# Kernel tuning notes

Measured on AMD Instinct MI355X. Metric: run time of the kernel, lower is better.

The kernel has to match this reference:

```python
import jax, jax.numpy as jnp
import numpy as np

# Model dims (match init_kwargs / Mamba2 defaults)
D_MODEL = 1024
D_STATE = 128
D_CONV = 4
EXPAND = 2
HEADDIM = 64
NGROUPS = 1
D_INNER = EXPAND * D_MODEL            # 2048
NHEADS = D_INNER // HEADDIM           # 32
D_IN_PROJ = 2 * D_INNER + 2 * NGROUPS * D_STATE + NHEADS  # 4384 (d_mlp == 0)
CONV_DIM = D_INNER + 2 * NGROUPS * D_STATE                 # 2304
BATCH = 2
SEQLEN = 512
EPS = 1e-5


def _silu(x):
    return x * jax.nn.sigmoid(x)


def setup_inputs() -> dict:
    key = jax.random.key(0)
    ks = jax.random.split(key, 8)
    u = jax.random.normal(ks[0], (BATCH, SEQLEN, D_MODEL), jnp.float32)
    W_in = jax.random.normal(ks[1], (D_IN_PROJ, D_MODEL), jnp.float32) * (D_MODEL ** -0.5)
    conv_w = jax.random.normal(ks[2], (CONV_DIM, 1, D_CONV), jnp.float32) * (D_CONV ** -0.5)
    conv_b = jnp.zeros((CONV_DIM,), jnp.float32)
    # dt_bias init as in the torch module (inverse-softplus of dt in [dt_min, dt_max])
    dt = jnp.exp(jax.random.uniform(ks[3], (NHEADS,), jnp.float32)
                 * (np.log(0.1) - np.log(0.001)) + np.log(0.001))
    dt = jnp.clip(dt, 1e-4, None)
    dt_bias = dt + jnp.log(-jnp.expm1(-dt))
    A_log = jnp.log(jax.random.uniform(ks[4], (NHEADS,), jnp.float32, minval=1.0, maxval=16.0))
    D_param = jnp.ones((NHEADS,), jnp.float32)
    norm_w = jnp.ones((D_INNER,), jnp.float32)
    W_out = jax.random.normal(ks[5], (D_MODEL, D_INNER), jnp.float32) * (D_INNER ** -0.5)
    return dict(u=u, W_in=W_in, conv_w=conv_w, conv_b=conv_b, dt_bias=dt_bias,
                A_log=A_log, D_param=D_param, norm_w=norm_w, W_out=W_out)


def reference(u, W_in, conv_w, conv_b, dt_bias, A_log, D_param, norm_w, W_out):
    B, L, _ = u.shape
    # in_proj (no bias): [B,L,d_in_proj]
    zxbcdt = jnp.einsum('bld,ed->ble', u, W_in)
    z = zxbcdt[..., :D_INNER]
    xBC = zxbcdt[..., D_INNER:D_INNER + CONV_DIM]
    dt = zxbcdt[..., D_INNER + CONV_DIM:]          # [B,L,H]

    # causal depthwise conv1d (pad left d_conv-1 == conv padding + slice in torch)
    xc = jnp.transpose(xBC, (0, 2, 1))             # [B,C,L]
    xc = jax.lax.conv_general_dilated(
        xc, conv_w, window_strides=(1,), padding=[(D_CONV - 1, 0)],
        dimension_numbers=('NCH', 'OIH', 'NCH'), feature_group_count=CONV_DIM)
    xc = xc + conv_b[None, :, None]
    xBC = _silu(jnp.transpose(xc, (0, 2, 1)))      # [B,L,C]

    x = xBC[..., :D_INNER].reshape(B, L, NHEADS, HEADDIM)
    Bv = xBC[..., D_INNER:D_INNER + NGROUPS * D_STATE].reshape(B, L, NGROUPS, D_STATE)
    Cv = xBC[..., D_INNER + NGROUPS * D_STATE:].reshape(B, L, NGROUPS, D_STATE)

    A = -jnp.exp(A_log)                            # [H]
    dt = jax.nn.softplus(dt + dt_bias)             # [B,L,H]

    def step(state, inp):
        dt_t, x_t, B_t, C_t = inp                  # [B,H],[B,H,P],[B,G,N],[B,G,N]
        dA = jnp.exp(dt_t * A)                     # [B,H]
        dBx = jnp.einsum('bh,bgn,bhp->bhpn', dt_t, B_t, x_t)
        state = state * dA[:, :, None, None] + dBx
        y = jnp.einsum('bhpn,bgn->bhp', state, C_t) + D_param[:, None] * x_t
        return state, y

    state0 = jnp.zeros((B, NHEADS, HEADDIM, D_STATE), u.dtype)
    xs = (jnp.moveaxis(dt, 1, 0), jnp.moveaxis(x, 1, 0),
          jnp.moveaxis(Bv, 1, 0), jnp.moveaxis(Cv, 1, 0))
    _, ys = jax.lax.scan(step, state0, xs)         # ys: [L,B,H,P]
    y = jnp.moveaxis(ys, 0, 1).reshape(B, L, D_INNER)

    # RMSNormGated, norm_before_gate=False: gate first, then rmsnorm
    yg = y * _silu(z)
    yn = yg * jax.lax.rsqrt(jnp.mean(yg * yg, axis=-1, keepdims=True) + EPS) * norm_w

    return jnp.einsum('bld,ed->ble', yn, W_out)    # out_proj, no bias
```

## Files before the change

kernel.cpp:

```cpp
#include <hip/hip_runtime.h>
#include <hip/hip_bf16.h>

#define D_MODEL   1024
#define D_STATE   128
#define D_INNER   2048
#define NHEADS    32
#define HEADDIM   64
#define D_IN_PROJ 4384
#define NPROJ_PAD 4480
#define CONV_DIM  2304
#define BATCH     2
#define SEQLEN    512
#define M_TOKENS  (BATCH*SEQLEN)
#define EPS       1e-5f
#define LC        64
#define NCH       (SEQLEN/LC)

typedef __bf16 bf16x8 __attribute__((ext_vector_type(8)));
typedef float  f32x4  __attribute__((ext_vector_type(4)));

__device__ __forceinline__ ushort f2bf(float f) {
  union { float f; unsigned int i; } v; v.f = f;
  unsigned int x = v.i;
  return (ushort)((x + 0x7fffu + ((x >> 16) & 1u)) >> 16);
}
__device__ __forceinline__ float bf2f(ushort u) {
  union { unsigned int i; float f; } v; v.i = ((unsigned int)u) << 16; return v.f;
}

__device__ __forceinline__ void gload_lds16u(const ushort* g, ushort* l) {
  __builtin_amdgcn_global_load_lds(
      (const __attribute__((address_space(1))) void*)g,
      (__attribute__((address_space(3))) void*)l, 16, 0, 0);
}

__device__ __forceinline__ void cvt8(const float* __restrict__ s,
                                     ushort* __restrict__ d, int i) {
  const float4 a = *(const float4*)(s + i);
  const float4 b = *(const float4*)(s + i + 4);
  uint4 v;
  v.x = (unsigned)f2bf(a.x) | ((unsigned)f2bf(a.y) << 16);
  v.y = (unsigned)f2bf(a.z) | ((unsigned)f2bf(a.w) << 16);
  v.z = (unsigned)f2bf(b.x) | ((unsigned)f2bf(b.y) << 16);
  v.w = (unsigned)f2bf(b.z) | ((unsigned)f2bf(b.w) << 16);
  *(uint4*)(d + i) = v;
}
__global__ __launch_bounds__(256) void cvt3z(const float* __restrict__ s0, ushort* __restrict__ d0, int n0,
                                             const float* __restrict__ s1, ushort* __restrict__ d1, int n1,
                                             const float* __restrict__ s2, ushort* __restrict__ d2, int n2,
                                             const float* __restrict__ nw,
                                             float* __restrict__ zout, int n3,
                                             float* __restrict__ zsum, int n4) {
  const int i = (blockIdx.x * 256 + threadIdx.x) * 8;
  if (i < n0)           cvt8(s0, d0, i);
  else if (i < n0 + n1) cvt8(s1, d1, i - n0);
  else if (i < n0 + n1 + n2) {
    const int j = i - n0 - n1;
    const int k = j & (D_INNER - 1);
    const float4 a = *(const float4*)(s2 + j);
    const float4 b = *(const float4*)(s2 + j + 4);
    const float4 wa = *(const float4*)(nw + k);
    const float4 wb = *(const float4*)(nw + k + 4);
    uint4 v;
    v.x = (unsigned)f2bf(a.x * wa.x) | ((unsigned)f2bf(a.y * wa.y) << 16);
    v.y = (unsigned)f2bf(a.z * wa.z) | ((unsigned)f2bf(a.w * wa.w) << 16);
    v.z = (unsigned)f2bf(b.x * wb.x) | ((unsigned)f2bf(b.y * wb.y) << 16);
    v.w = (unsigned)f2bf(b.z * wb.z) | ((unsigned)f2bf(b.w * wb.w) << 16);
    *(uint4*)(d2 + j) = v;
  } else if (i < n0 + n1 + n2 + n3) {
    const int j = i - n0 - n1 - n2;
    const float4 z = {0.f, 0.f, 0.f, 0.f};
    *(float4*)(zout + j) = z;
    *(float4*)(zout + j + 4) = z;
  } else if (i < n0 + n1 + n2 + n3 + n4) {
    const int j = i - n0 - n1 - n2 - n3;
    const float4 z = {0.f, 0.f, 0.f, 0.f};
    *(float4*)(zsum + j) = z;
    *(float4*)(zsum + j + 4) = z;
  }
}

template <int BM, int BN, int PK>
__global__ __launch_bounds__(256) void gemm_tile(const ushort* __restrict__ A,
                                                 const ushort* __restrict__ Bt,
                                                 ushort* __restrict__ C,
                                                 int Nreal, int K, int ldc) {
  constexpr int WM = BM / 2, WN = BN / 2, FM = WM / 16, FN = WN / 16;
  constexpr int LA = BM * 4 / 256, LB = BN * 4 / 256;
  __shared__ ushort As[PK * BM * 32];
  __shared__ ushort Bs[PK * BN * 32];
  const int tid = threadIdx.x, lane = tid & 63, wave = tid >> 6;
  const int r16 = lane & 15, q = lane >> 4;
  const int wm = wave & 1, wn = wave >> 1;
  const int m0 = blockIdx.y * BM, n0 = blockIdx.x * BN;

  f32x4 acc[FM][FN] = {};

  for (int k0 = 0; k0 < K; k0 += 32 * PK) {
    __syncthreads();
    #pragma unroll
    for (int pp = 0; pp < PK; ++pp) {
      #pragma unroll
      for (int it = 0; it < LA; ++it) {
        const int idx = it * 256 + tid;
        gload_lds16u(A + (size_t)(m0 + (idx >> 2)) * K + k0 + pp * 32 + (idx & 3) * 8,
                     As + pp * BM * 32 + (it * 256 + wave * 64) * 8);
      }
      #pragma unroll
      for (int it = 0; it < LB; ++it) {
        const int idx = it * 256 + tid;
        gload_lds16u(Bt + (size_t)(n0 + (idx >> 2)) * K + k0 + pp * 32 + (idx & 3) * 8,
                     Bs + pp * BN * 32 + (it * 256 + wave * 64) * 8);
      }
    }
    __syncthreads();

    #pragma unroll
    for (int pp = 0; pp < PK; ++pp) {
      bf16x8 af[FM], bfr[FN];
      #pragma unroll
      for (int i = 0; i < FM; ++i)
        af[i] = *(const bf16x8*)(const void*)(As + pp * BM * 32 + (wm * WM + i * 16 + r16) * 32 + q * 8);
      #pragma unroll
      for (int j = 0; j < FN; ++j)
        bfr[j] = *(const bf16x8*)(const void*)(Bs + pp * BN * 32 + (wn * WN + j * 16 + r16) * 32 + q * 8);
      #pragma unroll
      for (int i = 0; i < FM; ++i)
        #pragma unroll
        for (int j = 0; j < FN; ++j)
          acc[i][j] = __builtin_amdgcn_mfma_f32_16x16x32_bf16(af[i], bfr[j], acc[i][j], 0, 0, 0);
    }
  }

  #pragma unroll
  for (int i = 0; i < FM; ++i) {
    const int row = m0 + wm * WM + i * 16 + q * 4;
    #pragma unroll
    for (int j = 0; j < FN; ++j) {
      const int col = n0 + wn * WN + j * 16 + r16;
      if (col < Nreal) {
        #pragma unroll
        for (int r = 0; r < 4; ++r)
          C[(size_t)(row + r) * ldc + col] = f2bf(acc[i][j][r]);
      }
    }
  }
}

__global__ __launch_bounds__(256) void gemm_sk(const ushort* __restrict__ A,
                                               const ushort* __restrict__ Bt,
                                               float* __restrict__ C,
                                               const float* __restrict__ sumsq,
                                               int Khalf, int ldab, int ldc) {
  __shared__ ushort As[4 * 64 * 32];
  __shared__ ushort Bs[4 * 64 * 32];
  const int tid = threadIdx.x, lane = tid & 63, wave = tid >> 6;
  const int r16 = lane & 15, q = lane >> 4;
  const int wm = wave & 1, wn = wave >> 1;
  const int m0 = blockIdx.y * 64, n0 = blockIdx.x * 64;
  const int kb = blockIdx.z * Khalf;

  f32x4 acc[2][2] = {};
  for (int k0 = 0; k0 < Khalf; k0 += 128) {
    __syncthreads();
    #pragma unroll
    for (int pp = 0; pp < 4; ++pp) {
      gload_lds16u(A + (size_t)(m0 + (tid >> 2)) * ldab + kb + k0 + pp * 32 + (tid & 3) * 8,
                   As + pp * 64 * 32 + (tid & ~63) * 8);
      gload_lds16u(Bt + (size_t)(n0 + (tid >> 2)) * ldab + kb + k0 + pp * 32 + (tid & 3) * 8,
                   Bs + pp * 64 * 32 + (tid & ~63) * 8);
    }
    __syncthreads();

    #pragma unroll
    for (int pp = 0; pp < 4; ++pp) {
      bf16x8 af[2], bfr[2];
      #pragma unroll
      for (int i = 0; i < 2; ++i)
        af[i] = *(const bf16x8*)(const void*)(As + pp * 64 * 32 + (wm * 32 + i * 16 + r16) * 32 + q * 8);
      #pragma unroll
      for (int j = 0; j < 2; ++j)
        bfr[j] = *(const bf16x8*)(const void*)(Bs + pp * 64 * 32 + (wn * 32 + j * 16 + r16) * 32 + q * 8);
      #pragma unroll
      for (int i = 0; i < 2; ++i)
        #pragma unroll
        for (int j = 0; j < 2; ++j)
          acc[i][j] = __builtin_amdgcn_mfma_f32_16x16x32_bf16(af[i], bfr[j], acc[i][j], 0, 0, 0);
    }
  }

  #pragma unroll
  for (int i = 0; i < 2; ++i) {
    const int row = m0 + wm * 32 + i * 16 + q * 4;
    float rms[4];
    #pragma unroll
    for (int r = 0; r < 4; ++r)
      rms[r] = rsqrtf(sumsq[row + r] * (1.f / D_INNER) + EPS);
    #pragma unroll
    for (int j = 0; j < 2; ++j) {
      const int col = n0 + wn * 32 + j * 16 + r16;
      #pragma unroll
      for (int r = 0; r < 4; ++r)
        unsafeAtomicAdd(&C[(size_t)(row + r) * ldc + col], acc[i][j][r] * rms[r]);
    }
  }
}

__global__ __launch_bounds__(256) void conv_dt(const ushort* __restrict__ zx,
                                               const float* __restrict__ cw,
                                               const float* __restrict__ cb,
                                               ushort* __restrict__ xbc,
                                               const float* __restrict__ dt_bias,
                                               const float* __restrict__ A_log,
                                               float* __restrict__ dts,
                                               float* __restrict__ csum) {
  const int blk = blockIdx.x;
  if (blk < 1152) {
    const int g  = blk / 9;
    const int c  = (blk % 9) * 256 + threadIdx.x;
    const int b  = g >> 6;
    const int t0 = (g & 63) * 8;
    const float4 w4 = *(const float4*)(cw + c * 4);
    const float bias = cb[c];
    const ushort* col = zx + (size_t)(b * SEQLEN) * D_IN_PROJ + D_INNER + c;
    float win[11];
    #pragma unroll
    for (int k = 0; k < 11; ++k) {
      const int t = t0 - 3 + k;
      win[k] = (t >= 0) ? bf2f(col[(size_t)t * D_IN_PROJ]) : 0.f;
    }
    #pragma unroll
    for (int i = 0; i < 8; ++i) {
      float a = bias;
      a = fmaf(win[i],     w4.x, a);
      a = fmaf(win[i + 1], w4.y, a);
      a = fmaf(win[i + 2], w4.z, a);
      a = fmaf(win[i + 3], w4.w, a);
      const float s = a / (1.f + __expf(-a));
      xbc[(size_t)(b * SEQLEN + t0 + i) * CONV_DIM + c] = f2bf(s);
    }
  } else {
    const int bh = blk - 1152;
    const int b = bh >> 5, h = bh & 31;
    const int wave = threadIdx.x >> 6, lane = threadIdx.x & 63;
    const float dtb = dt_bias[h];
    const float An  = -__expf(A_log[h]);
    for (int cc = wave; cc < NCH; cc += 4) {
      const int t = cc * LC + lane;
      const float raw = bf2f(zx[(size_t)(b * SEQLEN + t) * D_IN_PROJ + (D_INNER + CONV_DIM) + h]) + dtb;
      const float sp = (raw > 20.f) ? raw : log1pf(__expf(raw));
      float x = sp * An;
      #pragma unroll
      for (int off = 1; off < 64; off <<= 1) {
        const float v = __shfl_up(x, off);
        if (lane >= off) x += v;
      }
      dts[(size_t)bh * SEQLEN + t]  = sp;
      csum[(size_t)bh * SEQLEN + t] = x;
    }
  }
}

__global__ __launch_bounds__(256) void chunk_intra(const ushort* __restrict__ xbc,
                                                   const float* __restrict__ dts,
                                                   const float* __restrict__ csum,
                                                   ushort* __restrict__ Yi,
                                                   ushort* __restrict__ dS) {
  const int blk = blockIdx.x;
  const int c = blk & 7, h = (blk >> 3) & 31, b = blk >> 8;
  const int bh = b * 32 + h;
  const int tid = threadIdx.x, lane = tid & 63, wave = tid >> 6;
  const int r16 = lane & 15, q = lane >> 4;

  __shared__ ushort Ml[64 * 72];
  __shared__ ushort Xt[64 * 72];
  __shared__ ushort Bw[128 * 72];
  __shared__ float dtl[LC], csl[LC];

  if (tid < LC) {
    dtl[tid] = dts[(size_t)bh * SEQLEN + c * LC + tid];
    csl[tid] = csum[(size_t)bh * SEQLEN + c * LC + tid];
  }
  __syncthreads();
  const float cs63 = csl[LC - 1];

  const ushort* rowbase = xbc + (size_t)(b * SEQLEN + c * LC) * CONV_DIM;
  const ushort* Cp = rowbase + (size_t)(wave * 16 + r16) * CONV_DIM + D_INNER + 128 + q * 8;
  const ushort* Bp = rowbase + (size_t)r16 * CONV_DIM + D_INNER + q * 8;
  f32x4 g[4] = {};
  #pragma unroll
  for (int kk = 0; kk < 4; ++kk) {
    const bf16x8 a = *(const bf16x8*)(const void*)(Cp + kk * 32);
    #pragma unroll
    for (int j = 0; j < 4; ++j) {
      const bf16x8 bb = *(const bf16x8*)(const void*)(Bp + (size_t)j * 16 * CONV_DIM + kk * 32);
      g[j] = __builtin_amdgcn_mfma_f32_16x16x32_bf16(a, bb, g[j], 0, 0, 0);
    }
  }
  float cst[4];
  #pragma unroll
  for (int r = 0; r < 4; ++r) cst[r] = csl[wave * 16 + q * 4 + r];
  #pragma unroll
  for (int j = 0; j < 4; ++j) {
    const int s = j * 16 + r16;
    const float ds_ = dtl[s], css = csl[s];
    #pragma unroll
    for (int r = 0; r < 4; ++r) {
      const int t = wave * 16 + q * 4 + r;
      const float v = (s <= t) ? g[j][r] * ds_ * __expf(cst[r] - css) : 0.f;
      Ml[t * 72 + s] = f2bf(v);
    }
  }

  const ushort* xb = rowbase + h * HEADDIM;
  #pragma unroll
  for (int i = 0; i < 16; ++i) {
    const int idx = i * 256 + tid;
    const int s = idx >> 6, p = idx & 63;
    Xt[p * 72 + s] = xb[(size_t)s * CONV_DIM + p];
  }
  const ushort* Bb = rowbase + D_INNER;
  #pragma unroll
  for (int i = 0; i < 32; ++i) {
    const int idx = i * 256 + tid;
    const int s = idx >> 7, n = idx & 127;
    const float w = dtl[s] * __expf(cs63 - csl[s]);
    Bw[n * 72 + s] = f2bf(bf2f(Bb[(size_t)s * CONV_DIM + n]) * w);
  }
  __syncthreads();

  f32x4 accY[4] = {};
  f32x4 accS[2][4] = {};
  #pragma unroll
  for (int kk = 0; kk < 2; ++kk) {
    const bf16x8 am = *(const bf16x8*)(const void*)(Ml + (wave * 16 + r16) * 72 + kk * 32 + q * 8);
    const bf16x8 a0 = *(const bf16x8*)(const void*)(Bw + (wave * 32 + r16) * 72 + kk * 32 + q * 8);
    const bf16x8 a1 = *(const bf16x8*)(const void*)(Bw + (wave * 32 + 16 + r16) * 72 + kk * 32 + q * 8);
    #pragma unroll
    for (int j = 0; j < 4; ++j) {
      const bf16x8 bx = *(const bf16x8*)(const void*)(Xt + (j * 16 + r16) * 72 + kk * 32 + q * 8);
      accY[j]    = __builtin_amdgcn_mfma_f32_16x16x32_bf16(am, bx, accY[j], 0, 0, 0);
      accS[0][j] = __builtin_amdgcn_mfma_f32_16x16x32_bf16(a0, bx, accS[0][j], 0, 0, 0);
      accS[1][j] = __builtin_amdgcn_mfma_f32_16x16x32_bf16(a1, bx, accS[1][j], 0, 0, 0);
    }
  }

  ushort* Yp = Yi + (size_t)blk * 4096;
  #pragma unroll
  for (int j = 0; j < 4; ++j)
    #pragma unroll
    for (int r = 0; r < 4; ++r)
      Yp[(wave * 16 + q * 4 + r) * 64 + j * 16 + r16] = f2bf(accY[j][r]);

  ushort* Sp = dS + (size_t)blk * 8192;
  #pragma unroll
  for (int u = 0; u < 2; ++u)
    #pragma unroll
    for (int j = 0; j < 4; ++j)
      #pragma unroll
      for (int r = 0; r < 4; ++r)
        Sp[(wave * 32 + u * 16 + q * 4 + r) * 64 + j * 16 + r16] = f2bf(accS[u][j][r]);
}

__global__ __launch_bounds__(256) void chunk_inter(const ushort* __restrict__ xbc,
                                                   const ushort* __restrict__ dS,
                                                   const ushort* __restrict__ Yi,
                                                   const ushort* __restrict__ zx,
                                                   const float* __restrict__ csum,
                                                   const float* __restrict__ Dp,
                                                   ushort* __restrict__ yn,
                                                   float* __restrict__ sumsq) {
  const int blk = blockIdx.x;
  const int c = blk & 7, h = (blk >> 3) & 31, b = blk >> 8;
  const int bh = b * 32 + h;
  const int tid = threadIdx.x, lane = tid & 63, wave = tid >> 6;
  const int r16 = lane & 15, q = lane >> 4;

  __shared__ ushort Stile[64 * 132];

  const int p  = tid & 63;
  const int n0 = (tid >> 6) * 32;
  float S[32] = {};
  float w = 1.f;
  for (int cp = c - 1; cp >= 0; --cp) {
    const ushort* dp = dS + ((size_t)bh * 8 + cp) * 8192 + (size_t)n0 * 64 + p;
    #pragma unroll
    for (int j = 0; j < 32; ++j)
      S[j] = fmaf(w, bf2f(dp[(size_t)j * 64]), S[j]);
    w *= __expf(csum[(size_t)bh * SEQLEN + cp * LC + (LC - 1)]);
  }
  #pragma unroll
  for (int j = 0; j < 16; ++j) {
    const unsigned v = (unsigned)f2bf(S[2 * j]) | ((unsigned)f2bf(S[2 * j + 1]) << 16);
    *(unsigned*)&Stile[p * 132 + n0 + 2 * j] = v;
  }
  __syncthreads();

  const ushort* rowbase = xbc + (size_t)(b * SEQLEN + c * LC) * CONV_DIM;
  const ushort* Cp = rowbase + (size_t)(wave * 16 + r16) * CONV_DIM + D_INNER + 128 + q * 8;
  f32x4 acc[4] = {};
  #pragma unroll
  for (int kk = 0; kk < 4; ++kk) {
    const bf16x8 a = *(const bf16x8*)(const void*)(Cp + kk * 32);
    #pragma unroll
    for (int j = 0; j < 4; ++j) {
      const bf16x8 bb = *(const bf16x8*)(const void*)(Stile + (j * 16 + r16) * 132 + kk * 32 + q * 8);
      acc[j] = __builtin_amdgcn_mfma_f32_16x16x32_bf16(a, bb, acc[j], 0, 0, 0);
    }
  }

  const float Dh = Dp[h];
  const ushort* Yp = Yi + (size_t)blk * 4096;
  float sc[4], ssq[4] = {0.f, 0.f, 0.f, 0.f};
  #pragma unroll
  for (int r = 0; r < 4; ++r)
    sc[r] = __expf(csum[(size_t)bh * SEQLEN + c * LC + wave * 16 + q * 4 + r]);
  #pragma unroll
  for (int j = 0; j < 4; ++j) {
    const int col = j * 16 + r16;
    #pragma unroll
    for (int r = 0; r < 4; ++r) {
      const int t = wave * 16 + q * 4 + r;
      const size_t row = (size_t)(b * SEQLEN + c * LC + t);
      const float xv = bf2f(xbc[row * CONV_DIM + h * HEADDIM + col]);
      const float yv = acc[j][r] * sc[r] + bf2f(Yp[t * 64 + col]) + Dh * xv;
      const float z  = bf2f(zx[row * D_IN_PROJ + h * HEADDIM + col]);
      const float yg = yv * (z / (1.f + __expf(-z)));
      yn[row * D_INNER + h * HEADDIM + col] = f2bf(yg);
      ssq[r] = fmaf(yg, yg, ssq[r]);
    }
  }
  #pragma unroll
  for (int o = 1; o < 16; o <<= 1) {
    #pragma unroll
    for (int r = 0; r < 4; ++r) ssq[r] += __shfl_xor(ssq[r], o);
  }
  if (r16 == 0) {
    #pragma unroll
    for (int r = 0; r < 4; ++r) {
      const int t = wave * 16 + q * 4 + r;
      unsafeAtomicAdd(&sumsq[b * SEQLEN + c * LC + t], ssq[r]);
    }
  }
}

extern "C" void kernel_launch(void* const* d_in, const int* in_sizes, int n_in,
                              void* d_out, int out_size, void* d_ws, size_t ws_size,
                              hipStream_t stream) {
  const float* u       = (const float*)d_in[0];
  const float* W_in    = (const float*)d_in[1];
  const float* conv_w  = (const float*)d_in[2];
  const float* conv_b  = (const float*)d_in[3];
  const float* dt_bias = (const float*)d_in[4];
  const float* A_log   = (const float*)d_in[5];
  const float* D_par   = (const float*)d_in[6];
  const float* norm_w  = (const float*)d_in[7];
  const float* W_out   = (const float*)d_in[8];
  float* out = (float*)d_out;

  char* ws = (char*)d_ws;
  ushort* zx      = (ushort*)ws;
  ushort* xbc     = (ushort*)(ws + 8978432);
  float*  sumsq   = (float*)(ws + 13697024);
  ushort* yn      = (ushort*)(ws + 13701120);
  ushort* u_bf    = (ushort*)(ws + 17895424);
  ushort* Win_bf  = (ushort*)(ws + 19992576);
  ushort* Yi      = (ushort*)(ws + 17895424);
  ushort* Wout_bf = (ushort*)(ws + 28971008);
  float*  dts     = (float*)(ws + 33165312);
  float*  csum    = (float*)(ws + 33296384);
  ushort* dS      = (ushort*)(ws + 33427456);

  const int n_u = M_TOKENS * D_MODEL, n_wi = D_IN_PROJ * D_MODEL, n_wo = D_MODEL * D_INNER;
  const int n_out = M_TOKENS * D_MODEL, n_ss = M_TOKENS;
  const int n_tot = n_u + n_wi + n_wo + n_out + n_ss;
  cvt3z<<<(n_tot + 2047) / 2048, 256, 0, stream>>>(
      u, u_bf, n_u, W_in, Win_bf, n_wi, W_out, Wout_bf, n_wo, norm_w,
      out, n_out, sumsq, n_ss);

  gemm_tile<128, 64, 4><<<dim3(NPROJ_PAD / 64, M_TOKENS / 128), 256, 0, stream>>>(
      u_bf, Win_bf, zx, D_IN_PROJ, D_MODEL, D_IN_PROJ);
  conv_dt<<<1152 + 64, 256, 0, stream>>>(zx, conv_w, conv_b, xbc,
                                         dt_bias, A_log, dts, csum);

  chunk_intra<<<BATCH * NHEADS * NCH, 256, 0, stream>>>(xbc, dts, csum, Yi, dS);
  chunk_inter<<<BATCH * NHEADS * NCH, 256, 0, stream>>>(xbc, dS, Yi, zx,
                                                        csum, D_par, yn, sumsq);

  gemm_sk<<<dim3(D_MODEL / 64, M_TOKENS / 64, 2), 256, 0, stream>>>(
      yn, Wout_bf, out, sumsq, D_INNER / 2, D_INNER, D_MODEL);
}
```

Baseline: 164.2 us.

## Double-buffer LDS staging in both GEMM kernels to overlap loads with MFMA

Both the in-projection and out-projection GEMMs switch from a single-stage LDS fill (4 sub-tiles of K=32, two barriers per step) to a two-buffer ping-pong of 2 sub-tiles each. The next K=64 slab is issued into the other buffer before the MFMAs run on the current one, and each iteration needs only one barrier. The aim is to hide global-to-LDS latency behind compute. LDS footprint stays the same, but each iteration covers half as much K, so there are twice as many loop trips.

```diff
diff --git a/kernel.cpp b/kernel.cpp
--- a/kernel.cpp
+++ b/kernel.cpp
@@ -80,15 +80,15 @@
   }
 }
 
-template <int BM, int BN, int PK>
+template <int BM, int BN>
 __global__ __launch_bounds__(256) void gemm_tile(const ushort* __restrict__ A,
                                                  const ushort* __restrict__ Bt,
                                                  ushort* __restrict__ C,
                                                  int Nreal, int K, int ldc) {
   constexpr int WM = BM / 2, WN = BN / 2, FM = WM / 16, FN = WN / 16;
   constexpr int LA = BM * 4 / 256, LB = BN * 4 / 256;
-  __shared__ ushort As[PK * BM * 32];
-  __shared__ ushort Bs[PK * BN * 32];
+  __shared__ ushort As[2 * 2 * BM * 32];
+  __shared__ ushort Bs[2 * 2 * BN * 32];
   const int tid = threadIdx.x, lane = tid & 63, wave = tid >> 6;
   const int r16 = lane & 15, q = lane >> 4;
   const int wm = wave & 1, wn = wave >> 1;
@@ -96,34 +96,39 @@
 
   f32x4 acc[FM][FN] = {};
 
-  for (int k0 = 0; k0 < K; k0 += 32 * PK) {
-    __syncthreads();
-    #pragma unroll
-    for (int pp = 0; pp < PK; ++pp) {
+  auto stage = [&](int buf, int k0) {
+    #pragma unroll
+    for (int pp = 0; pp < 2; ++pp) {
       #pragma unroll
       for (int it = 0; it < LA; ++it) {
         const int idx = it * 256 + tid;
         gload_lds16u(A + (size_t)(m0 + (idx >> 2)) * K + k0 + pp * 32 + (idx & 3) * 8,
-                     As + pp * BM * 32 + (it * 256 + wave * 64) * 8);
+                     As + (buf * 2 + pp) * BM * 32 + (it * 256 + wave * 64) * 8);
       }
       #pragma unroll
       for (int it = 0; it < LB; ++it) {
         const int idx = it * 256 + tid;
         gload_lds16u(Bt + (size_t)(n0 + (idx >> 2)) * K + k0 + pp * 32 + (idx & 3) * 8,
-                     Bs + pp * BN * 32 + (it * 256 + wave * 64) * 8);
+                     Bs + (buf * 2 + pp) * BN * 32 + (it * 256 + wave * 64) * 8);
       }
     }
+  };
+
+  const int NK = K / 64;
+  stage(0, 0);
+  for (int k = 0; k < NK; ++k) {
+    const int buf = k & 1;
     __syncthreads();
-
-    #pragma unroll
-    for (int pp = 0; pp < PK; ++pp) {
+    if (k + 1 < NK) stage(buf ^ 1, (k + 1) * 64);
+    #pragma unroll
+    for (int pp = 0; pp < 2; ++pp) {
       bf16x8 af[FM], bfr[FN];
       #pragma unroll
       for (int i = 0; i < FM; ++i)
-        af[i] = *(const bf16x8*)(const void*)(As + pp * BM * 32 + (wm * WM + i * 16 + r16) * 32 + q * 8);
+        af[i] = *(const bf16x8*)(const void*)(As + (buf * 2 + pp) * BM * 32 + (wm * WM + i * 16 + r16) * 32 + q * 8);
       #pragma unroll
       for (int j = 0; j < FN; ++j)
-        bfr[j] = *(const bf16x8*)(const void*)(Bs + pp * BN * 32 + (wn * WN + j * 16 + r16) * 32 + q * 8);
+        bfr[j] = *(const bf16x8*)(const void*)(Bs + (buf * 2 + pp) * BN * 32 + (wn * WN + j * 16 + r16) * 32 + q * 8);
       #pragma unroll
       for (int i = 0; i < FM; ++i)
         #pragma unroll
@@ -152,8 +157,8 @@
                                                float* __restrict__ C,
                                                const float* __restrict__ sumsq,
                                                int Khalf, int ldab, int ldc) {
-  __shared__ ushort As[4 * 64 * 32];
-  __shared__ ushort Bs[4 * 64 * 32];
+  __shared__ ushort As[2 * 2 * 64 * 32];
+  __shared__ ushort Bs[2 * 2 * 64 * 32];
   const int tid = threadIdx.x, lane = tid & 63, wave = tid >> 6;
   const int r16 = lane & 15, q = lane >> 4;
   const int wm = wave & 1, wn = wave >> 1;
@@ -161,26 +166,32 @@
   const int kb = blockIdx.z * Khalf;
 
   f32x4 acc[2][2] = {};
-  for (int k0 = 0; k0 < Khalf; k0 += 128) {
+
+  auto stage = [&](int buf, int k0) {
+    #pragma unroll
+    for (int pp = 0; pp < 2; ++pp) {
+      gload_lds16u(A + (size_t)(m0 + (tid >> 2)) * ldab + kb + k0 + pp * 32 + (tid & 3) * 8,
+                   As + (buf * 2 + pp) * 64 * 32 + (tid & ~63) * 8);
+      gload_lds16u(Bt + (size_t)(n0 + (tid >> 2)) * ldab + kb + k0 + pp * 32 + (tid & 3) * 8,
+                   Bs + (buf * 2 + pp) * 64 * 32 + (tid & ~63) * 8);
+    }
+  };
+
+  const int NK = Khalf / 64;
+  stage(0, 0);
+  for (int k = 0; k < NK; ++k) {
+    const int buf = k & 1;
     __syncthreads();
-    #pragma unroll
-    for (int pp = 0; pp < 4; ++pp) {
-      gload_lds16u(A + (size_t)(m0 + (tid >> 2)) * ldab + kb + k0 + pp * 32 + (tid & 3) * 8,
-                   As + pp * 64 * 32 + (tid & ~63) * 8);
-      gload_lds16u(Bt + (size_t)(n0 + (tid >> 2)) * ldab + kb + k0 + pp * 32 + (tid & 3) * 8,
-                   Bs + pp * 64 * 32 + (tid & ~63) * 8);
-    }
-    __syncthreads();
-
-    #pragma unroll
-    for (int pp = 0; pp < 4; ++pp) {
+    if (k + 1 < NK) stage(buf ^ 1, (k + 1) * 64);
+    #pragma unroll
+    for (int pp = 0; pp < 2; ++pp) {
       bf16x8 af[2], bfr[2];
       #pragma unroll
       for (int i = 0; i < 2; ++i)
-        af[i] = *(const bf16x8*)(const void*)(As + pp * 64 * 32 + (wm * 32 + i * 16 + r16) * 32 + q * 8);
+        af[i] = *(const bf16x8*)(const void*)(As + (buf * 2 + pp) * 64 * 32 + (wm * 32 + i * 16 + r16) * 32 + q * 8);
       #pragma unroll
       for (int j = 0; j < 2; ++j)
-        bfr[j] = *(const bf16x8*)(const void*)(Bs + pp * 64 * 32 + (wn * 32 + j * 16 + r16) * 32 + q * 8);
+        bfr[j] = *(const bf16x8*)(const void*)(Bs + (buf * 2 + pp) * 64 * 32 + (wn * 32 + j * 16 + r16) * 32 + q * 8);
       #pragma unroll
       for (int i = 0; i < 2; ++i)
         #pragma unroll
@@ -478,7 +489,7 @@
       u, u_bf, n_u, W_in, Win_bf, n_wi, W_out, Wout_bf, n_wo, norm_w,
       out, n_out, sumsq, n_ss);
 
-  gemm_tile<128, 64, 4><<<dim3(NPROJ_PAD / 64, M_TOKENS / 128), 256, 0, stream>>>(
+  gemm_tile<128, 64><<<dim3(NPROJ_PAD / 64, M_TOKENS / 128), 256, 0, stream>>>(
       u_bf, Win_bf, zx, D_IN_PROJ, D_MODEL, D_IN_PROJ);
   conv_dt<<<1152 + 64, 256, 0, stream>>>(zx, conv_w, conv_b, xbc,
                                          dt_bias, A_log, dts, csum);
```

Measured after the change: 165.1 us. Within noise of the previous version (+0.5%).
